# Kernel optimization log

Hardware: AMD Instinct MI355X
Metric: run time of the kernel (lower is better)

## Reference

```python
import math
import jax, jax.numpy as jnp
import numpy as np

B, L = 64, 25
FEAT, HEADS, LAYERS = 128, 8, 2
USER_N, POI_N, CAT_N = 5000, 10000, 400


def _autocorr(q, k, v):
    # q,k,v: [B,L,H,E] ; training-mode AutoCorrelation (self.training=True)
    Lq = q.shape[1]
    qp = jnp.transpose(q, (0, 2, 3, 1))  # [B,H,E,L]
    kp = jnp.transpose(k, (0, 2, 3, 1))
    vp = jnp.transpose(v, (0, 2, 3, 1))
    qf = jnp.fft.rfft(qp, axis=-1)
    kf = jnp.fft.rfft(kp, axis=-1)
    corr = jnp.fft.irfft(qf * jnp.conj(kf), n=Lq, axis=-1)  # [B,H,E,L]
    top_k = int(1 * math.log(Lq))  # factor=1 -> 3 for L=25
    mean_value = corr.mean(axis=(1, 2))  # [B,L]
    _, index = jax.lax.top_k(mean_value.mean(axis=0), top_k)  # [K], shared across batch
    weights = mean_value[:, index]  # [B,K]
    tmp_corr = jax.nn.softmax(weights, axis=-1)
    # roll(values, -delay) == gather at (t + delay) mod L
    gidx = (jnp.arange(Lq)[None, :] + index[:, None]) % Lq  # [K,L]
    patterns = vp[..., gidx]  # [B,H,E,K,L]
    agg = jnp.einsum('bhekl,bk->bhel', patterns, tmp_corr)  # weighted delay aggregation
    return jnp.transpose(agg, (0, 3, 1, 2))  # [B,L,H,E]


def _ac_layer(qx, kx, vx, w, b):
    # w: [4, d, d] torch-layout [out,in] for (q,k,v,out) projections; b: [4, d]
    Bq, Lq, d = qx.shape
    q = (qx @ w[0].T + b[0]).reshape(Bq, Lq, HEADS, -1)
    k = (kx @ w[1].T + b[1]).reshape(Bq, kx.shape[1], HEADS, -1)
    v = (vx @ w[2].T + b[2]).reshape(Bq, vx.shape[1], HEADS, -1)
    out = _autocorr(q, k, v).reshape(Bq, Lq, -1)
    return out @ w[3].T + b[3]


def setup_inputs() -> dict:
    key = jax.random.key(0)
    ks = jax.random.split(key, 16)
    d = FEAT
    inp = {
        'user': jax.random.randint(ks[0], (B, L), 0, USER_N),
        'poi': jax.random.randint(ks[1], (B, L), 0, POI_N),
        'cat': jax.random.randint(ks[2], (B, L), 0, CAT_N),
        'lat': jax.random.normal(ks[3], (B, L), jnp.float32),
        'lon': jax.random.normal(ks[4], (B, L), jnp.float32),
        'tod': jax.random.randint(ks[5], (B, L), 0, 24),
        'dow': jax.random.randint(ks[6], (B, L), 0, 7),
        'unixtime': jax.random.normal(ks[7], (B, L), jnp.float32),
        'user_emb': jax.random.normal(ks[8], (USER_N, d), jnp.float32) * 0.02,
        'poi_emb': jax.random.normal(ks[9], (POI_N, d), jnp.float32) * 0.02,
        'cat_emb': jax.random.normal(ks[10], (CAT_N, d), jnp.float32) * 0.02,
        'tod_emb': jax.random.normal(ks[11], (24, d), jnp.float32) * 0.02,
        'dow_emb': jax.random.normal(ks[12], (7, d), jnp.float32) * 0.02,
        'user_embc': jax.random.normal(jax.random.fold_in(ks[8], 1), (USER_N, d), jnp.float32) * 0.02,
        'tod_embc': jax.random.normal(jax.random.fold_in(ks[11], 1), (24, d), jnp.float32) * 0.02,
        'dow_embc': jax.random.normal(jax.random.fold_in(ks[12], 1), (7, d), jnp.float32) * 0.02,
        # W[layer, module(poi,cat,xpoi,xcat), proj(q,k,v,o), out, in]
        'W': jax.random.normal(ks[13], (LAYERS, 4, 4, d, d), jnp.float32) * (1.0 / math.sqrt(d)),
        'Bv': jnp.zeros((LAYERS, 4, 4, d), jnp.float32),
        'value_w': jax.random.normal(ks[14], (1, L), jnp.float32) * 0.1,
        'value_b': jnp.zeros((1,), jnp.float32),
        'distance_matrix': jax.random.uniform(ks[15], (POI_N, POI_N), jnp.float32) * 10.0,
    }
    return inp


def reference(user, poi, cat, lat, lon, tod, dow, unixtime,
              user_emb, poi_emb, cat_emb, tod_emb, dow_emb,
              user_embc, tod_embc, dow_embc,
              W, Bv, value_w, value_b, distance_matrix):
    x = user_emb[user] + poi_emb[poi] + tod_emb[tod] + dow_emb[dow]        # [B,L,d]
    xc = user_embc[user] + cat_emb[cat] + tod_embc[tod] + dow_embc[dow]   # [B,L,d]

    interval_dis = distance_matrix[poi]  # [B,L,P] row gather == index_select loop
    interval = jnp.exp(-interval_dis / (interval_dis.max() - interval_dis.min()))

    out, outc = x, xc
    for i in range(LAYERS):
        out = _ac_layer(out, out, out, W[i, 0], Bv[i, 0])
        outc = _ac_layer(outc, outc, outc, W[i, 1], Bv[i, 1])
        out = _ac_layer(out, outc, outc, W[i, 2], Bv[i, 2])
        outc = _ac_layer(outc, out, out, W[i, 3], Bv[i, 3])

    attn = jnp.einsum('pd,bld->bpl', poi_emb, out) * jnp.transpose(interval, (0, 2, 1))
    attn_cat = jnp.einsum('cd,bld->bcl', cat_emb, outc)
    pre_poi = (attn @ value_w.T + value_b)[..., 0]      # [B,P]
    pre_cat = (attn_cat @ value_w.T + value_b)[..., 0]  # [B,C]
    return pre_poi, pre_cat
```

## Files before the change

### kernel.cpp

```cpp
#include <hip/hip_runtime.h>

#define BB 64
#define LL 25
#define DD 128
#define BL 1600
#define POI_N 10000
#define CAT_N 400
#define NBLK 150
#define NGRP 8

__device__ __forceinline__ void gridbar(unsigned* __restrict__ bar, int id)
{
    __syncthreads();
    if (threadIdx.x == 0) {
        unsigned* base = bar + id * (NGRP * 32);
        __hip_atomic_fetch_add(base + (blockIdx.x & (NGRP - 1)) * 32, 1u,
                               __ATOMIC_RELEASE, __HIP_MEMORY_SCOPE_AGENT);
        for (;;) {
            unsigned s = 0;
#pragma unroll
            for (int g = 0; g < NGRP; g++)
                s += __hip_atomic_load(base + g * 32, __ATOMIC_RELAXED,
                                       __HIP_MEMORY_SCOPE_AGENT);
            if (s >= NBLK) break;
            __builtin_amdgcn_s_sleep(1);
        }
        __builtin_amdgcn_fence(__ATOMIC_ACQUIRE, "agent");
    }
    __syncthreads();
}

__global__ __launch_bounds__(256) void minmax_kernel(
    const int* __restrict__ poi, const float* __restrict__ Dm, unsigned* __restrict__ mm)
{
    int bl = blockIdx.x;
    const float4* r = (const float4*)(Dm + (size_t)poi[bl] * POI_N);
    float mx = -1e30f, mn = 1e30f;
    for (int i = threadIdx.x; i < POI_N / 4; i += 256) {
        float4 v4 = r[i];
        mx = fmaxf(mx, fmaxf(fmaxf(v4.x, v4.y), fmaxf(v4.z, v4.w)));
        mn = fminf(mn, fminf(fminf(v4.x, v4.y), fminf(v4.z, v4.w)));
    }
    for (int off = 32; off > 0; off >>= 1) {
        mx = fmaxf(mx, __shfl_down(mx, off));
        mn = fminf(mn, __shfl_down(mn, off));
    }
    __shared__ float smx[4], smn[4];
    int lid = threadIdx.x & 63, wid = threadIdx.x >> 6;
    if (lid == 0) { smx[wid] = mx; smn[wid] = mn; }
    __syncthreads();
    if (threadIdx.x == 0) {
        mx = fmaxf(fmaxf(smx[0], smx[1]), fmaxf(smx[2], smx[3]));
        mn = fminf(fminf(smn[0], smn[1]), fminf(smn[2], smn[3]));
        atomicMax(&mm[0], __float_as_uint(mx));
        atomicMax(&mm[1], ~__float_as_uint(mn));
    }
}

__global__ __launch_bounds__(256) void persist_kernel(
    const int* __restrict__ user, const int* __restrict__ poi, const int* __restrict__ cat,
    const int* __restrict__ tod, const int* __restrict__ dow,
    const float* __restrict__ ue, const float* __restrict__ pe, const float* __restrict__ ce,
    const float* __restrict__ te, const float* __restrict__ de,
    const float* __restrict__ uec, const float* __restrict__ tec, const float* __restrict__ dec,
    const float* __restrict__ W, const float* __restrict__ Bv,
    const float* __restrict__ vw, const float* __restrict__ vbp,
    float* __restrict__ O0, float* __restrict__ C0, float* __restrict__ O1, float* __restrict__ C1,
    float* __restrict__ Qb, float* __restrict__ Kb, float* __restrict__ Vb,
    float* __restrict__ MV,
    unsigned* __restrict__ bar,
    float* __restrict__ out_cat)
{
    __shared__ __align__(16) char smem_raw[51712];
    float (*sS)[132] = reinterpret_cast<float(*)[132]>(smem_raw);
    float (*sWc)[68] = reinterpret_cast<float(*)[68]>(smem_raw + 16896);
    float* csq       = reinterpret_cast<float*>(smem_raw);
    float* csk       = reinterpret_cast<float*>(smem_raw + 12800);
    float (*crb)[4]  = reinterpret_cast<float(*)[4]>(smem_raw + 25600);

    __shared__ float sbm[LL];
    __shared__ int   sidx[3];
    __shared__ float stc[BB][3];
    __shared__ float yv[DD];
    __shared__ float svw[LL];

    int bx = blockIdx.x, t = threadIdx.x;

    for (int i = bx * 256 + t; i < 51200; i += NBLK * 256) {
        int bl = i >> 5, c = (i & 31) << 2;
        int u = user[bl], p = poi[bl], cc = cat[bl], td = tod[bl], dw = dow[bl];
        float4 a0 = *(const float4*)(ue + u * DD + c);
        float4 a1 = *(const float4*)(pe + p * DD + c);
        float4 a2 = *(const float4*)(te + td * DD + c);
        float4 a3 = *(const float4*)(de + dw * DD + c);
        float4 x;
        x.x = a0.x + a1.x + a2.x + a3.x; x.y = a0.y + a1.y + a2.y + a3.y;
        x.z = a0.z + a1.z + a2.z + a3.z; x.w = a0.w + a1.w + a2.w + a3.w;
        *(float4*)(O0 + bl * DD + c) = x;
        float4 b0 = *(const float4*)(uec + u * DD + c);
        float4 b1 = *(const float4*)(ce + cc * DD + c);
        float4 b2 = *(const float4*)(tec + td * DD + c);
        float4 b3 = *(const float4*)(dec + dw * DD + c);
        float4 xc;
        xc.x = b0.x + b1.x + b2.x + b3.x; xc.y = b0.y + b1.y + b2.y + b3.y;
        xc.z = b0.z + b1.z + b2.z + b3.z; xc.w = b0.w + b1.w + b2.w + b3.w;
        *(float4*)(C0 + bl * DD + c) = xc;
    }
    gridbar(bar, 0);

    float* bufs[4] = {O0, C0, O1, C1};
    const int qsel[8] = {0, 1, 2, 3, 0, 1, 2, 3};
    const int ksel[8] = {0, 1, 3, 0, 0, 1, 3, 0};
    const int dsel[8] = {2, 3, 0, 1, 2, 3, 0, 1};
    int bid = 1;

#pragma unroll 1
    for (int ci = 0; ci < 8; ++ci) {
        const float* qx  = bufs[qsel[ci]];
        const float* kx  = bufs[ksel[ci]];
        float*       dst = bufs[dsel[ci]];
        const float* Wb  = W  + (size_t)ci * 4 * DD * DD;
        const float* Bb  = Bv + (size_t)ci * 4 * DD;

        {
            int r = bx / 50, tile = bx % 50;
            const float* src  = (r == 0) ? qx : kx;
            const float* Wm   = Wb + r * DD * DD;
            const float* bias = Bb + r * DD;
            float* pdst       = (r == 0) ? Qb : (r == 1 ? Kb : Vb);
            int mbase = tile * 32;

            for (int i = t; i < 32 * 32; i += 256) {
                int m = i >> 5, c = (i & 31) << 2;
                *(float4*)&sS[m][c] = *(const float4*)(src + (mbase + m) * DD + c);
            }
            __syncthreads();
            int nh = t & 31, mg = t >> 5;
            float acc[4][4] = {};
            for (int kb = 0; kb < 128; kb += 64) {
                for (int i = t; i < 128 * 16; i += 256) {
                    int n = i >> 4, c = (i & 15) << 2;
                    *(float4*)&sWc[n][c] = *(const float4*)(Wm + n * DD + kb + c);
                }
                __syncthreads();
#pragma unroll 4
                for (int kk = 0; kk < 64; kk += 4) {
                    float4 a[4], w[4];
#pragma unroll
                    for (int i2 = 0; i2 < 4; i2++) a[i2] = *(const float4*)&sS[mg * 4 + i2][kb + kk];
#pragma unroll
                    for (int j = 0; j < 4; j++) w[j] = *(const float4*)&sWc[nh + 32 * j][kk];
#pragma unroll
                    for (int i2 = 0; i2 < 4; i2++)
#pragma unroll
                        for (int j = 0; j < 4; j++)
                            acc[i2][j] += a[i2].x * w[j].x + a[i2].y * w[j].y +
                                          a[i2].z * w[j].z + a[i2].w * w[j].w;
                }
                __syncthreads();
            }
#pragma unroll
            for (int i2 = 0; i2 < 4; i2++) {
                int m = mbase + mg * 4 + i2;
#pragma unroll
                for (int j = 0; j < 4; j++) {
                    int n = nh + 32 * j;
                    pdst[m * DD + n] = acc[i2][j] + bias[n];
                }
            }
        }
        gridbar(bar, bid++);

        if (bx < BB) {
            int b = bx;
            for (int i = t; i < 800; i += 256) {
                int c = i << 2;
                *(float4*)&csq[c] = *(const float4*)(Qb + b * LL * DD + c);
                *(float4*)&csk[c] = *(const float4*)(Kb + b * LL * DD + c);
            }
            __syncthreads();
            int lid = t & 63, wid = t >> 6;
            for (int tau = 0; tau < LL; tau++) {
                float s = 0.f;
                for (int e = t; e < 800; e += 256) {
                    int srow = e >> 5, dc = (e & 31) << 2;
                    int qrow = srow + tau; if (qrow >= LL) qrow -= LL;
                    float4 a = *(const float4*)&csq[qrow * DD + dc];
                    float4 g = *(const float4*)&csk[srow * DD + dc];
                    s += a.x * g.x + a.y * g.y + a.z * g.z + a.w * g.w;
                }
                for (int off = 32; off > 0; off >>= 1) s += __shfl_down(s, off);
                if (lid == 0) crb[tau][wid] = s;
            }
            __syncthreads();
            if (t < LL)
                MV[b * LL + t] = (crb[t][0] + crb[t][1] + crb[t][2] + crb[t][3]) * (1.0f / 128.0f);
        }
        gridbar(bar, bid++);

        if (bx < 50) {
            int mbase = bx * 32;
            if (t < LL) {
                float s = 0.f;
                for (int b2 = 0; b2 < BB; b2++) s += MV[b2 * LL + t];
                sbm[t] = s;
            }
            __syncthreads();
            if (t == 0) {
                float loc[LL];
                for (int i = 0; i < LL; i++) loc[i] = sbm[i];
                for (int j = 0; j < 3; j++) {
                    int bi = 0; float bvv = loc[0];
                    for (int i = 1; i < LL; i++) if (loc[i] > bvv) { bvv = loc[i]; bi = i; }
                    sidx[j] = bi; loc[bi] = -1e30f;
                }
            }
            __syncthreads();
            if (t < BB) {
                float w0 = MV[t * LL + sidx[0]];
                float w1 = MV[t * LL + sidx[1]];
                float w2 = MV[t * LL + sidx[2]];
                float m = fmaxf(w0, fmaxf(w1, w2));
                float e0 = expf(w0 - m), e1 = expf(w1 - m), e2 = expf(w2 - m);
                float inv = 1.0f / (e0 + e1 + e2);
                stc[t][0] = e0 * inv; stc[t][1] = e1 * inv; stc[t][2] = e2 * inv;
            }
            __syncthreads();
            int i0 = sidx[0], i1 = sidx[1], i2x = sidx[2];
            const float* Wm   = Wb + 3 * DD * DD;
            const float* bias = Bb + 3 * DD;

            for (int i = t; i < 32 * 32; i += 256) {
                int m = i >> 5, c = (i & 31) << 2;
                int row = mbase + m;
                int b = row / LL, l = row - b * LL;
                int l0 = l + i0;  if (l0 >= LL) l0 -= LL;
                int l1 = l + i1;  if (l1 >= LL) l1 -= LL;
                int l2 = l + i2x; if (l2 >= LL) l2 -= LL;
                float w0 = stc[b][0], w1 = stc[b][1], w2 = stc[b][2];
                float4 v0 = *(const float4*)(Vb + (b * LL + l0) * DD + c);
                float4 v1 = *(const float4*)(Vb + (b * LL + l1) * DD + c);
                float4 v2 = *(const float4*)(Vb + (b * LL + l2) * DD + c);
                float4 a;
                a.x = w0 * v0.x + w1 * v1.x + w2 * v2.x;
                a.y = w0 * v0.y + w1 * v1.y + w2 * v2.y;
                a.z = w0 * v0.z + w1 * v1.z + w2 * v2.z;
                a.w = w0 * v0.w + w1 * v1.w + w2 * v2.w;
                *(float4*)&sS[m][c] = a;
            }
            __syncthreads();
            int nh = t & 31, mg = t >> 5;
            float acc[4][4] = {};
            for (int kb = 0; kb < 128; kb += 64) {
                for (int i = t; i < 128 * 16; i += 256) {
                    int n = i >> 4, c = (i & 15) << 2;
                    *(float4*)&sWc[n][c] = *(const float4*)(Wm + n * DD + kb + c);
                }
                __syncthreads();
#pragma unroll 4
                for (int kk = 0; kk < 64; kk += 4) {
                    float4 a[4], w[4];
#pragma unroll
                    for (int ii = 0; ii < 4; ii++) a[ii] = *(const float4*)&sS[mg * 4 + ii][kb + kk];
#pragma unroll
                    for (int j = 0; j < 4; j++) w[j] = *(const float4*)&sWc[nh + 32 * j][kk];
#pragma unroll
                    for (int ii = 0; ii < 4; ii++)
#pragma unroll
                        for (int j = 0; j < 4; j++)
                            acc[ii][j] += a[ii].x * w[j].x + a[ii].y * w[j].y +
                                          a[ii].z * w[j].z + a[ii].w * w[j].w;
                }
                __syncthreads();
            }
#pragma unroll
            for (int ii = 0; ii < 4; ii++) {
                int m = mbase + mg * 4 + ii;
#pragma unroll
                for (int j = 0; j < 4; j++) {
                    int n = nh + 32 * j;
                    dst[m * DD + n] = acc[ii][j] + bias[n];
                }
            }
        }
        gridbar(bar, bid++);
    }

    if (bx < BB) {
        int b = bx;
        if (t < LL) svw[t] = vw[t];
        __syncthreads();
        if (t < DD) {
            float s = 0.f;
            for (int l = 0; l < LL; l++) s += svw[l] * C0[(b * LL + l) * DD + t];
            yv[t] = s;
        }
        __syncthreads();
        float vb = vbp[0];
        for (int c = t; c < CAT_N; c += 256) {
            float s = 0.f;
            for (int d = 0; d < DD; d += 4) {
                float4 ce4 = *(const float4*)(ce + c * DD + d);
                s += ce4.x * yv[d] + ce4.y * yv[d + 1] + ce4.z * yv[d + 2] + ce4.w * yv[d + 3];
            }
            out_cat[b * CAT_N + c] = s + vb;
        }
    }
}

__global__ __launch_bounds__(256) void prepoi_kernel(
    const float* __restrict__ outp, const float* __restrict__ poi_emb,
    const int* __restrict__ poi_idx, const float* __restrict__ Dm,
    const unsigned* __restrict__ mm, const float* __restrict__ vw,
    const float* __restrict__ vbp, float* __restrict__ dstp)
{
    int b = blockIdx.y;
    int pbase = blockIdx.x << 7;
    __shared__ float sO[LL][132];
    __shared__ float sPc[128][68];
    __shared__ float sS[LL][132];
    __shared__ float svw[LL];
    __shared__ int srow[LL];
    __shared__ float red[128];
    int t = threadIdx.x;

    for (int i = t; i < 800; i += 256) {
        int l = i >> 5, c = (i & 31) << 2;
        *(float4*)&sO[l][c] = *(const float4*)(outp + (b * LL + l) * DD + c);
    }
    if (t < LL) { svw[t] = vw[t]; srow[t] = poi_idx[b * LL + t]; }
    __syncthreads();

    int nh = t & 31, mg = t >> 5;
    float acc[4][4] = {};
    for (int kb = 0; kb < 128; kb += 64) {
        for (int i = t; i < 128 * 16; i += 256) {
            int p = i >> 4, c = (i & 15) << 2;
            float4 val = {0.f, 0.f, 0.f, 0.f};
            if (pbase + p < POI_N) val = *(const float4*)(poi_emb + (pbase + p) * DD + kb + c);
            *(float4*)&sPc[p][c] = val;
        }
        __syncthreads();
#pragma unroll 4
        for (int kk = 0; kk < 64; kk += 4) {
            float4 a0 = *(const float4*)&sO[mg][kb + kk];
            float4 a1 = *(const float4*)&sO[mg + 8][kb + kk];
            float4 a2 = *(const float4*)&sO[mg + 16][kb + kk];
            float4 a3 = {0.f, 0.f, 0.f, 0.f};
            if (mg == 0) a3 = *(const float4*)&sO[24][kb + kk];
#pragma unroll
            for (int j = 0; j < 4; j++) {
                float4 p4 = *(const float4*)&sPc[nh + 32 * j][kk];
                acc[j][0] += p4.x * a0.x + p4.y * a0.y + p4.z * a0.z + p4.w * a0.w;
                acc[j][1] += p4.x * a1.x + p4.y * a1.y + p4.z * a1.z + p4.w * a1.w;
                acc[j][2] += p4.x * a2.x + p4.y * a2.y + p4.z * a2.z + p4.w * a2.w;
                acc[j][3] += p4.x * a3.x + p4.y * a3.y + p4.z * a3.z + p4.w * a3.w;
            }
        }
        __syncthreads();
    }
#pragma unroll
    for (int j = 0; j < 4; j++) {
        int pl = nh + 32 * j;
        sS[mg][pl]      = acc[j][0];
        sS[mg + 8][pl]  = acc[j][1];
        sS[mg + 16][pl] = acc[j][2];
        if (mg == 0) sS[24][pl] = acc[j][3];
    }
    __syncthreads();

    float gmax = __uint_as_float(mm[0]);
    float gmin = __uint_as_float(~mm[1]);
    float ninv = -1.0f / (gmax - gmin);
    int pp = t & 127, half = t >> 7;
    int p = pbase + pp;
    float s = 0.f;
    if (p < POI_N) {
        int l0 = half ? 13 : 0, l1 = half ? 25 : 13;
        for (int l = l0; l < l1; l++) {
            float dv = Dm[(size_t)srow[l] * POI_N + p];
            s += svw[l] * expf(dv * ninv) * sS[l][pp];
        }
    }
    if (half) red[pp] = s;
    __syncthreads();
    if (!half && p < POI_N)
        dstp[(size_t)b * POI_N + p] = s + red[pp] + vbp[0];
}

extern "C" void kernel_launch(void* const* d_in, const int* in_sizes, int n_in,
                              void* d_out, int out_size, void* d_ws, size_t ws_size,
                              hipStream_t stream)
{
    const int*   user = (const int*)d_in[0];
    const int*   poi  = (const int*)d_in[1];
    const int*   cat  = (const int*)d_in[2];
    const int*   tod  = (const int*)d_in[5];
    const int*   dow  = (const int*)d_in[6];
    const float* ue   = (const float*)d_in[8];
    const float* pe   = (const float*)d_in[9];
    const float* ce   = (const float*)d_in[10];
    const float* te   = (const float*)d_in[11];
    const float* de   = (const float*)d_in[12];
    const float* uec  = (const float*)d_in[13];
    const float* tec  = (const float*)d_in[14];
    const float* dec  = (const float*)d_in[15];
    const float* W    = (const float*)d_in[16];
    const float* Bv   = (const float*)d_in[17];
    const float* vw   = (const float*)d_in[18];
    const float* vb   = (const float*)d_in[19];
    const float* Dm   = (const float*)d_in[20];

    float* ws = (float*)d_ws;
    float* O0 = ws;
    float* C0 = ws + 204800;
    float* O1 = ws + 409600;
    float* C1 = ws + 614400;
    float* Q  = ws + 819200;
    float* Kb = ws + 1024000;
    float* V  = ws + 1228800;
    float* MV = ws + 1433600;
    unsigned* BAR = (unsigned*)(ws + 1435200);
    unsigned* MM  = BAR + 25 * NGRP * 32;

    float* out_poi = (float*)d_out;
    float* out_cat = out_poi + BB * POI_N;

    hipMemsetAsync(BAR, 0, (25 * NGRP * 32 + 2) * sizeof(unsigned), stream);

    minmax_kernel<<<BL, 256, 0, stream>>>(poi, Dm, MM);

    persist_kernel<<<NBLK, 256, 0, stream>>>(
        user, poi, cat, tod, dow, ue, pe, ce, te, de, uec, tec, dec,
        W, Bv, vw, vb, O0, C0, O1, C1, Q, Kb, V, MV, BAR, out_cat);

    prepoi_kernel<<<dim3(79, BB), 256, 0, stream>>>(O0, pe, poi, Dm, MM, vw, vb, out_poi);
}
```

Before: 1.180 ms.

## Assign one block per batch row, replacing three grid barriers with one sync

The persistent kernel now runs one block per batch row (64 blocks), computing the QKV projections, autocorrelation, aggregation and output projection locally. This leaves a single cross-block exchange per layer call, needed for the batch-shared top-k. It replaces three grid-wide barriers per stage over 150 blocks, but uses fewer CUs and repeats the weight loads in every block. The atomic min/max is also swapped for a two-kernel reduction, and the sync drops its explicit acquire fence in favour of atomic loads.

```diff
diff --git a/kernel.cpp b/kernel.cpp
--- a/kernel.cpp
+++ b/kernel.cpp
@@ -6,32 +6,32 @@
 #define BL 1600
 #define POI_N 10000
 #define CAT_N 400
-#define NBLK 150
-#define NGRP 8
-
-__device__ __forceinline__ void gridbar(unsigned* __restrict__ bar, int id)
+#define NBLK 64
+#define NSH 8
+
+__device__ __forceinline__ void mvsync(unsigned* __restrict__ cnt, int ci, int bx)
 {
     __syncthreads();
     if (threadIdx.x == 0) {
-        unsigned* base = bar + id * (NGRP * 32);
-        __hip_atomic_fetch_add(base + (blockIdx.x & (NGRP - 1)) * 32, 1u,
+        unsigned* base = cnt + ci * (NSH * 32);
+        __hip_atomic_fetch_add(base + (bx & (NSH - 1)) * 32, 1u,
                                __ATOMIC_RELEASE, __HIP_MEMORY_SCOPE_AGENT);
         for (;;) {
             unsigned s = 0;
 #pragma unroll
-            for (int g = 0; g < NGRP; g++)
+            for (int g = 0; g < NSH; g++)
                 s += __hip_atomic_load(base + g * 32, __ATOMIC_RELAXED,
                                        __HIP_MEMORY_SCOPE_AGENT);
             if (s >= NBLK) break;
             __builtin_amdgcn_s_sleep(1);
         }
-        __builtin_amdgcn_fence(__ATOMIC_ACQUIRE, "agent");
-    }
-    __syncthreads();
-}
-
-__global__ __launch_bounds__(256) void minmax_kernel(
-    const int* __restrict__ poi, const float* __restrict__ Dm, unsigned* __restrict__ mm)
+    }
+    __syncthreads();
+}
+
+__global__ __launch_bounds__(256) void minmax1_kernel(
+    const int* __restrict__ poi, const float* __restrict__ Dm,
+    float* __restrict__ mxA, float* __restrict__ mnA)
 {
     int bl = blockIdx.x;
     const float4* r = (const float4*)(Dm + (size_t)poi[bl] * POI_N);
@@ -50,10 +50,30 @@
     if (lid == 0) { smx[wid] = mx; smn[wid] = mn; }
     __syncthreads();
     if (threadIdx.x == 0) {
-        mx = fmaxf(fmaxf(smx[0], smx[1]), fmaxf(smx[2], smx[3]));
-        mn = fminf(fminf(smn[0], smn[1]), fminf(smn[2], smn[3]));
-        atomicMax(&mm[0], __float_as_uint(mx));
-        atomicMax(&mm[1], ~__float_as_uint(mn));
+        mxA[bl] = fmaxf(fmaxf(smx[0], smx[1]), fmaxf(smx[2], smx[3]));
+        mnA[bl] = fminf(fminf(smn[0], smn[1]), fminf(smn[2], smn[3]));
+    }
+}
+
+__global__ __launch_bounds__(256) void minmax2_kernel(
+    const float* __restrict__ mxA, const float* __restrict__ mnA, float* __restrict__ mmf)
+{
+    float mx = -1e30f, mn = 1e30f;
+    for (int i = threadIdx.x; i < BL; i += 256) {
+        mx = fmaxf(mx, mxA[i]);
+        mn = fminf(mn, mnA[i]);
+    }
+    for (int off = 32; off > 0; off >>= 1) {
+        mx = fmaxf(mx, __shfl_down(mx, off));
+        mn = fminf(mn, __shfl_down(mn, off));
+    }
+    __shared__ float smx[4], smn[4];
+    int lid = threadIdx.x & 63, wid = threadIdx.x >> 6;
+    if (lid == 0) { smx[wid] = mx; smn[wid] = mn; }
+    __syncthreads();
+    if (threadIdx.x == 0) {
+        mmf[0] = fmaxf(fmaxf(smx[0], smx[1]), fmaxf(smx[2], smx[3]));
+        mmf[1] = fminf(fminf(smn[0], smn[1]), fminf(smn[2], smn[3]));
     }
 }
 
@@ -66,28 +86,68 @@
     const float* __restrict__ W, const float* __restrict__ Bv,
     const float* __restrict__ vw, const float* __restrict__ vbp,
     float* __restrict__ O0, float* __restrict__ C0, float* __restrict__ O1, float* __restrict__ C1,
-    float* __restrict__ Qb, float* __restrict__ Kb, float* __restrict__ Vb,
-    float* __restrict__ MV,
-    unsigned* __restrict__ bar,
+    float* __restrict__ Qg, float* __restrict__ Kg, float* __restrict__ Vg,
+    unsigned* __restrict__ MVu,
+    unsigned* __restrict__ cnt,
     float* __restrict__ out_cat)
 {
-    __shared__ __align__(16) char smem_raw[51712];
-    float (*sS)[132] = reinterpret_cast<float(*)[132]>(smem_raw);
-    float (*sWc)[68] = reinterpret_cast<float(*)[68]>(smem_raw + 16896);
-    float* csq       = reinterpret_cast<float*>(smem_raw);
-    float* csk       = reinterpret_cast<float*>(smem_raw + 12800);
-    float (*crb)[4]  = reinterpret_cast<float(*)[4]>(smem_raw + 25600);
-
+    __shared__ float sA[LL][132];
+    __shared__ float sB[LL][132];
+    __shared__ float sWc[128][68];
+    __shared__ float crb[LL][4];
+    __shared__ float smv[LL];
+    __shared__ float pbm[8][LL];
     __shared__ float sbm[LL];
     __shared__ int   sidx[3];
-    __shared__ float stc[BB][3];
+    __shared__ float sw3[3];
     __shared__ float yv[DD];
     __shared__ float svw[LL];
 
     int bx = blockIdx.x, t = threadIdx.x;
-
-    for (int i = bx * 256 + t; i < 51200; i += NBLK * 256) {
-        int bl = i >> 5, c = (i & 31) << 2;
+    int b = bx;
+    int nh = t & 31, mg = t >> 5;
+
+    auto gemm = [&](const float (&A)[LL][132], const float* Wm,
+                    const float* bias, float* gdst) {
+        float acc[4][4] = {};
+        for (int kb = 0; kb < 128; kb += 64) {
+            for (int i = t; i < 128 * 16; i += 256) {
+                int n = i >> 4, c = (i & 15) << 2;
+                *(float4*)&sWc[n][c] = *(const float4*)(Wm + n * DD + kb + c);
+            }
+            __syncthreads();
+#pragma unroll 4
+            for (int kk = 0; kk < 64; kk += 4) {
+                float4 a0 = *(const float4*)&A[mg][kb + kk];
+                float4 a1 = *(const float4*)&A[mg + 8][kb + kk];
+                float4 a2 = *(const float4*)&A[mg + 16][kb + kk];
+                float4 a3 = {0.f, 0.f, 0.f, 0.f};
+                if (mg == 0) a3 = *(const float4*)&A[24][kb + kk];
+#pragma unroll
+                for (int j = 0; j < 4; j++) {
+                    float4 p4 = *(const float4*)&sWc[nh + 32 * j][kk];
+                    acc[j][0] += p4.x * a0.x + p4.y * a0.y + p4.z * a0.z + p4.w * a0.w;
+                    acc[j][1] += p4.x * a1.x + p4.y * a1.y + p4.z * a1.z + p4.w * a1.w;
+                    acc[j][2] += p4.x * a2.x + p4.y * a2.y + p4.z * a2.z + p4.w * a2.w;
+                    acc[j][3] += p4.x * a3.x + p4.y * a3.y + p4.z * a3.z + p4.w * a3.w;
+                }
+            }
+            __syncthreads();
+        }
+#pragma unroll
+        for (int j = 0; j < 4; j++) {
+            int n = nh + 32 * j;
+            float bv = bias[n];
+            gdst[(mg) * DD + n]      = acc[j][0] + bv;
+            gdst[(mg + 8) * DD + n]  = acc[j][1] + bv;
+            gdst[(mg + 16) * DD + n] = acc[j][2] + bv;
+            if (mg == 0) gdst[24 * DD + n] = acc[j][3] + bv;
+        }
+    };
+
+    for (int i = t; i < 800; i += 256) {
+        int l = i >> 5, c = (i & 31) << 2;
+        int bl = b * LL + l;
         int u = user[bl], p = poi[bl], cc = cat[bl], td = tod[bl], dw = dow[bl];
         float4 a0 = *(const float4*)(ue + u * DD + c);
         float4 a1 = *(const float4*)(pe + p * DD + c);
@@ -106,188 +166,129 @@
         xc.z = b0.z + b1.z + b2.z + b3.z; xc.w = b0.w + b1.w + b2.w + b3.w;
         *(float4*)(C0 + bl * DD + c) = xc;
     }
-    gridbar(bar, 0);
+    __syncthreads();
 
     float* bufs[4] = {O0, C0, O1, C1};
     const int qsel[8] = {0, 1, 2, 3, 0, 1, 2, 3};
     const int ksel[8] = {0, 1, 3, 0, 0, 1, 3, 0};
     const int dsel[8] = {2, 3, 0, 1, 2, 3, 0, 1};
-    int bid = 1;
+
+    float* Qb = Qg + b * LL * DD;
+    float* Kb = Kg + b * LL * DD;
+    float* Vb = Vg + b * LL * DD;
 
 #pragma unroll 1
     for (int ci = 0; ci < 8; ++ci) {
-        const float* qx  = bufs[qsel[ci]];
-        const float* kx  = bufs[ksel[ci]];
-        float*       dst = bufs[dsel[ci]];
+        const float* qx  = bufs[qsel[ci]] + b * LL * DD;
+        const float* kx  = bufs[ksel[ci]] + b * LL * DD;
+        float*       dst = bufs[dsel[ci]] + b * LL * DD;
         const float* Wb  = W  + (size_t)ci * 4 * DD * DD;
         const float* Bb  = Bv + (size_t)ci * 4 * DD;
 
+        for (int i = t; i < 800; i += 256) {
+            int l = i >> 5, c = (i & 31) << 2;
+            *(float4*)&sA[l][c] = *(const float4*)(qx + l * DD + c);
+            *(float4*)&sB[l][c] = *(const float4*)(kx + l * DD + c);
+        }
+        __syncthreads();
+
+        gemm(sA, Wb,               Bb,          Qb);
+        gemm(sB, Wb + 1 * DD * DD, Bb + DD,     Kb);
+        gemm(sB, Wb + 2 * DD * DD, Bb + 2 * DD, Vb);
+
+        __syncthreads();
+        for (int i = t; i < 800; i += 256) {
+            int l = i >> 5, c = (i & 31) << 2;
+            *(float4*)&sA[l][c] = *(const float4*)(Qb + l * DD + c);
+            *(float4*)&sB[l][c] = *(const float4*)(Kb + l * DD + c);
+        }
+        __syncthreads();
+
+        int lid = t & 63, wid = t >> 6;
+        for (int tau = 0; tau < LL; tau++) {
+            float s = 0.f;
+            for (int e = t; e < 800; e += 256) {
+                int srow = e >> 5, dc = (e & 31) << 2;
+                int qrow = srow + tau; if (qrow >= LL) qrow -= LL;
+                float4 a = *(const float4*)&sA[qrow][dc];
+                float4 g = *(const float4*)&sB[srow][dc];
+                s += a.x * g.x + a.y * g.y + a.z * g.z + a.w * g.w;
+            }
+            for (int off = 32; off > 0; off >>= 1) s += __shfl_down(s, off);
+            if (lid == 0) crb[tau][wid] = s;
+        }
+        __syncthreads();
+        if (t < LL) {
+            float v = (crb[t][0] + crb[t][1] + crb[t][2] + crb[t][3]) * (1.0f / 128.0f);
+            smv[t] = v;
+            __hip_atomic_store(&MVu[ci * BL + b * LL + t], __float_as_uint(v),
+                               __ATOMIC_RELAXED, __HIP_MEMORY_SCOPE_AGENT);
+        }
+
+        mvsync(cnt, ci, bx);
+
+        if (t < 200) {
+            int g = t / LL, tau = t - g * LL;
+            float s = 0.f;
+#pragma unroll
+            for (int k2 = 0; k2 < 8; k2++) {
+                int b2 = g * 8 + k2;
+                s += __uint_as_float(__hip_atomic_load(&MVu[ci * BL + b2 * LL + tau],
+                                                       __ATOMIC_RELAXED,
+                                                       __HIP_MEMORY_SCOPE_AGENT));
+            }
+            pbm[g][tau] = s;
+        }
+        __syncthreads();
+        if (t < LL) {
+            float s = 0.f;
+#pragma unroll
+            for (int g = 0; g < 8; g++) s += pbm[g][t];
+            sbm[t] = s;
+        }
+        __syncthreads();
+        if (t == 0) {
+            float loc[LL];
+            for (int i = 0; i < LL; i++) loc[i] = sbm[i];
+            for (int j = 0; j < 3; j++) {
+                int bi = 0; float bvv = loc[0];
+                for (int i = 1; i < LL; i++) if (loc[i] > bvv) { bvv = loc[i]; bi = i; }
+                sidx[j] = bi; loc[bi] = -1e30f;
+            }
+            float w0 = smv[sidx[0]], w1 = smv[sidx[1]], w2 = smv[sidx[2]];
+            float m = fmaxf(w0, fmaxf(w1, w2));
+            float e0 = expf(w0 - m), e1 = expf(w1 - m), e2 = expf(w2 - m);
+            float inv = 1.0f / (e0 + e1 + e2);
+            sw3[0] = e0 * inv; sw3[1] = e1 * inv; sw3[2] = e2 * inv;
+        }
+        __syncthreads();
+
         {
-            int r = bx / 50, tile = bx % 50;
-            const float* src  = (r == 0) ? qx : kx;
-            const float* Wm   = Wb + r * DD * DD;
-            const float* bias = Bb + r * DD;
-            float* pdst       = (r == 0) ? Qb : (r == 1 ? Kb : Vb);
-            int mbase = tile * 32;
-
-            for (int i = t; i < 32 * 32; i += 256) {
-                int m = i >> 5, c = (i & 31) << 2;
-                *(float4*)&sS[m][c] = *(const float4*)(src + (mbase + m) * DD + c);
-            }
-            __syncthreads();
-            int nh = t & 31, mg = t >> 5;
-            float acc[4][4] = {};
-            for (int kb = 0; kb < 128; kb += 64) {
-                for (int i = t; i < 128 * 16; i += 256) {
-                    int n = i >> 4, c = (i & 15) << 2;
-                    *(float4*)&sWc[n][c] = *(const float4*)(Wm + n * DD + kb + c);
-                }
-                __syncthreads();
-#pragma unroll 4
-                for (int kk = 0; kk < 64; kk += 4) {
-                    float4 a[4], w[4];
-#pragma unroll
-                    for (int i2 = 0; i2 < 4; i2++) a[i2] = *(const float4*)&sS[mg * 4 + i2][kb + kk];
-#pragma unroll
-                    for (int j = 0; j < 4; j++) w[j] = *(const float4*)&sWc[nh + 32 * j][kk];
-#pragma unroll
-                    for (int i2 = 0; i2 < 4; i2++)
-#pragma unroll
-                        for (int j = 0; j < 4; j++)
-                            acc[i2][j] += a[i2].x * w[j].x + a[i2].y * w[j].y +
-                                          a[i2].z * w[j].z + a[i2].w * w[j].w;
-                }
-                __syncthreads();
-            }
-#pragma unroll
-            for (int i2 = 0; i2 < 4; i2++) {
-                int m = mbase + mg * 4 + i2;
-#pragma unroll
-                for (int j = 0; j < 4; j++) {
-                    int n = nh + 32 * j;
-                    pdst[m * DD + n] = acc[i2][j] + bias[n];
-                }
-            }
-        }
-        gridbar(bar, bid++);
-
-        if (bx < BB) {
-            int b = bx;
+            int i0 = sidx[0], i1 = sidx[1], i2x = sidx[2];
+            float w0 = sw3[0], w1 = sw3[1], w2 = sw3[2];
             for (int i = t; i < 800; i += 256) {
-                int c = i << 2;
-                *(float4*)&csq[c] = *(const float4*)(Qb + b * LL * DD + c);
-                *(float4*)&csk[c] = *(const float4*)(Kb + b * LL * DD + c);
-            }
-            __syncthreads();
-            int lid = t & 63, wid = t >> 6;
-            for (int tau = 0; tau < LL; tau++) {
-                float s = 0.f;
-                for (int e = t; e < 800; e += 256) {
-                    int srow = e >> 5, dc = (e & 31) << 2;
-                    int qrow = srow + tau; if (qrow >= LL) qrow -= LL;
-                    float4 a = *(const float4*)&csq[qrow * DD + dc];
-                    float4 g = *(const float4*)&csk[srow * DD + dc];
-                    s += a.x * g.x + a.y * g.y + a.z * g.z + a.w * g.w;
-                }
-                for (int off = 32; off > 0; off >>= 1) s += __shfl_down(s, off);
-                if (lid == 0) crb[tau][wid] = s;
-            }
-            __syncthreads();
-            if (t < LL)
-                MV[b * LL + t] = (crb[t][0] + crb[t][1] + crb[t][2] + crb[t][3]) * (1.0f / 128.0f);
-        }
-        gridbar(bar, bid++);
-
-        if (bx < 50) {
-            int mbase = bx * 32;
-            if (t < LL) {
-                float s = 0.f;
-                for (int b2 = 0; b2 < BB; b2++) s += MV[b2 * LL + t];
-                sbm[t] = s;
-            }
-            __syncthreads();
-            if (t == 0) {
-                float loc[LL];
-                for (int i = 0; i < LL; i++) loc[i] = sbm[i];
-                for (int j = 0; j < 3; j++) {
-                    int bi = 0; float bvv = loc[0];
-                    for (int i = 1; i < LL; i++) if (loc[i] > bvv) { bvv = loc[i]; bi = i; }
-                    sidx[j] = bi; loc[bi] = -1e30f;
-                }
-            }
-            __syncthreads();
-            if (t < BB) {
-                float w0 = MV[t * LL + sidx[0]];
-                float w1 = MV[t * LL + sidx[1]];
-                float w2 = MV[t * LL + sidx[2]];
-                float m = fmaxf(w0, fmaxf(w1, w2));
-                float e0 = expf(w0 - m), e1 = expf(w1 - m), e2 = expf(w2 - m);
-                float inv = 1.0f / (e0 + e1 + e2);
-                stc[t][0] = e0 * inv; stc[t][1] = e1 * inv; stc[t][2] = e2 * inv;
-            }
-            __syncthreads();
-            int i0 = sidx[0], i1 = sidx[1], i2x = sidx[2];
-            const float* Wm   = Wb + 3 * DD * DD;
-            const float* bias = Bb + 3 * DD;
-
-            for (int i = t; i < 32 * 32; i += 256) {
-                int m = i >> 5, c = (i & 31) << 2;
-                int row = mbase + m;
-                int b = row / LL, l = row - b * LL;
+                int l = i >> 5, c = (i & 31) << 2;
                 int l0 = l + i0;  if (l0 >= LL) l0 -= LL;
                 int l1 = l + i1;  if (l1 >= LL) l1 -= LL;
                 int l2 = l + i2x; if (l2 >= LL) l2 -= LL;
-                float w0 = stc[b][0], w1 = stc[b][1], w2 = stc[b][2];
-                float4 v0 = *(const float4*)(Vb + (b * LL + l0) * DD + c);
-                float4 v1 = *(const float4*)(Vb + (b * LL + l1) * DD + c);
-                float4 v2 = *(const float4*)(Vb + (b * LL + l2) * DD + c);
+                float4 v0 = *(const float4*)(Vb + l0 * DD + c);
+                float4 v1 = *(const float4*)(Vb + l1 * DD + c);
+                float4 v2 = *(const float4*)(Vb + l2 * DD + c);
                 float4 a;
                 a.x = w0 * v0.x + w1 * v1.x + w2 * v2.x;
                 a.y = w0 * v0.y + w1 * v1.y + w2 * v2.y;
                 a.z = w0 * v0.z + w1 * v1.z + w2 * v2.z;
                 a.w = w0 * v0.w + w1 * v1.w + w2 * v2.w;
-                *(float4*)&sS[m][c] = a;
+                *(float4*)&sA[l][c] = a;
             }
             __syncthreads();
-            int nh = t & 31, mg = t >> 5;
-            float acc[4][4] = {};
-            for (int kb = 0; kb < 128; kb += 64) {
-                for (int i = t; i < 128 * 16; i += 256) {
-                    int n = i >> 4, c = (i & 15) << 2;
-                    *(float4*)&sWc[n][c] = *(const float4*)(Wm + n * DD + kb + c);
-                }
-                __syncthreads();
-#pragma unroll 4
-                for (int kk = 0; kk < 64; kk += 4) {
-                    float4 a[4], w[4];
-#pragma unroll
-                    for (int ii = 0; ii < 4; ii++) a[ii] = *(const float4*)&sS[mg * 4 + ii][kb + kk];
-#pragma unroll
-                    for (int j = 0; j < 4; j++) w[j] = *(const float4*)&sWc[nh + 32 * j][kk];
-#pragma unroll
-                    for (int ii = 0; ii < 4; ii++)
-#pragma unroll
-                        for (int j = 0; j < 4; j++)
-                            acc[ii][j] += a[ii].x * w[j].x + a[ii].y * w[j].y +
-                                          a[ii].z * w[j].z + a[ii].w * w[j].w;
-                }
-                __syncthreads();
-            }
-#pragma unroll
-            for (int ii = 0; ii < 4; ii++) {
-                int m = mbase + mg * 4 + ii;
-#pragma unroll
-                for (int j = 0; j < 4; j++) {
-                    int n = nh + 32 * j;
-                    dst[m * DD + n] = acc[ii][j] + bias[n];
-                }
-            }
-        }
-        gridbar(bar, bid++);
-    }
-
-    if (bx < BB) {
-        int b = bx;
+        }
+
+        gemm(sA, Wb + 3 * DD * DD, Bb + 3 * DD, dst);
+        __syncthreads();
+    }
+
+    {
         if (t < LL) svw[t] = vw[t];
         __syncthreads();
         if (t < DD) {
@@ -311,7 +312,7 @@
 __global__ __launch_bounds__(256) void prepoi_kernel(
     const float* __restrict__ outp, const float* __restrict__ poi_emb,
     const int* __restrict__ poi_idx, const float* __restrict__ Dm,
-    const unsigned* __restrict__ mm, const float* __restrict__ vw,
+    const float* __restrict__ mmf, const float* __restrict__ vw,
     const float* __restrict__ vbp, float* __restrict__ dstp)
 {
     int b = blockIdx.y;
@@ -369,8 +370,8 @@
     }
     __syncthreads();
 
-    float gmax = __uint_as_float(mm[0]);
-    float gmin = __uint_as_float(~mm[1]);
+    float gmax = mmf[0];
+    float gmin = mmf[1];
     float ninv = -1.0f / (gmax - gmin);
     int pp = t & 127, half = t >> 7;
     int p = pbase + pp;
@@ -416,23 +417,26 @@
     float* C0 = ws + 204800;
     float* O1 = ws + 409600;
     float* C1 = ws + 614400;
-    float* Q  = ws + 819200;
-    float* Kb = ws + 1024000;
-    float* V  = ws + 1228800;
-    float* MV = ws + 1433600;
-    unsigned* BAR = (unsigned*)(ws + 1435200);
-    unsigned* MM  = BAR + 25 * NGRP * 32;
+    float* Qg = ws + 819200;
+    float* Kg = ws + 1024000;
+    float* Vg = ws + 1228800;
+    unsigned* MVu = (unsigned*)(ws + 1433600);
+    float* mxA = ws + 1446400;
+    float* mnA = ws + 1448000;
+    unsigned* CNT = (unsigned*)(ws + 1449600);
+    float* MMF = ws + 1449600 + 2048;
 
     float* out_poi = (float*)d_out;
     float* out_cat = out_poi + BB * POI_N;
 
-    hipMemsetAsync(BAR, 0, (25 * NGRP * 32 + 2) * sizeof(unsigned), stream);
-
-    minmax_kernel<<<BL, 256, 0, stream>>>(poi, Dm, MM);
+    hipMemsetAsync(CNT, 0, 8 * NSH * 32 * sizeof(unsigned), stream);
+
+    minmax1_kernel<<<BL, 256, 0, stream>>>(poi, Dm, mxA, mnA);
+    minmax2_kernel<<<1, 256, 0, stream>>>(mxA, mnA, MMF);
 
     persist_kernel<<<NBLK, 256, 0, stream>>>(
         user, poi, cat, tod, dow, ue, pe, ce, te, de, uec, tec, dec,
-        W, Bv, vw, vb, O0, C0, O1, C1, Q, Kb, V, MV, BAR, out_cat);
-
-    prepoi_kernel<<<dim3(79, BB), 256, 0, stream>>>(O0, pe, poi, Dm, MM, vw, vb, out_poi);
-}
+        W, Bv, vw, vb, O0, C0, O1, C1, Qg, Kg, Vg, MVu, CNT, out_cat);
+
+    prepoi_kernel<<<dim3(79, BB), 256, 0, stream>>>(O0, pe, poi, Dm, MMF, vw, vb, out_poi);
+}
```

After: 1.212 ms. 1.03x slower.
